# Performance work log

Measured on AMD Instinct MI355X. Metric: run time of the kernel, lower is better.

The kernel has to match this reference:

```python
import jax, jax.numpy as jnp
import numpy as np

EXPERT_NUM = 8
TOPK = 2
N_EMBD = 768
D_FF = 3072
B, S = 2, 1024
T = B * S


def setup_inputs() -> dict:
    key = jax.random.key(0)
    ks = jax.random.split(key, 6)
    x = jax.random.normal(ks[0], (B, S, N_EMBD), dtype=jnp.float32)
    # gumbel noise, matching gumbel_noise(n, k) in the torch module
    u = jax.random.uniform(ks[1], (T, EXPERT_NUM), dtype=jnp.float32,
                           minval=1e-6, maxval=1.0 - 1e-6)
    noise = -jnp.log(-jnp.log(u))
    router_w = jax.random.normal(ks[2], (EXPERT_NUM, N_EMBD), dtype=jnp.float32) * (N_EMBD ** -0.5)
    w1 = jax.random.normal(ks[3], (EXPERT_NUM, N_EMBD, D_FF), dtype=jnp.float32) * (N_EMBD ** -0.5)
    b1 = jnp.zeros((EXPERT_NUM, D_FF), dtype=jnp.float32)
    w2 = jax.random.normal(ks[4], (EXPERT_NUM, D_FF, N_EMBD), dtype=jnp.float32) * (D_FF ** -0.5)
    b2 = jnp.zeros((EXPERT_NUM, N_EMBD), dtype=jnp.float32)
    return {"x": x, "noise": noise, "router_w": router_w,
            "w1": w1, "b1": b1, "w2": w2, "b2": b2}


def reference(x, noise, router_w, w1, b1, w2, b2):
    d = x.shape[-1]
    xs = x.reshape(-1, d)                                   # [T, d]
    gate_logits = xs @ router_w.T + noise                   # [T, E]
    # topk_exp > 1 branch: topk first, then softmax over the k kept logits
    weights, selected = jax.lax.top_k(gate_logits, TOPK)    # [T, k]
    weights = jax.nn.softmax(weights.astype(jnp.float32), axis=1).astype(x.dtype)
    out = jnp.zeros_like(xs)
    for e in range(EXPERT_NUM):
        # combine weight of expert e per token (0 where not selected)
        w_e = jnp.sum(jnp.where(selected == e, weights, 0.0), axis=1)  # [T]
        h = jax.nn.gelu(xs @ w1[e] + b1[e])                 # [T, d_ff]
        y = h @ w2[e] + b2[e]                               # [T, d]
        out = out + w_e[:, None] * y
    return out.reshape(x.shape)
```

## Files before the change

kernel.cpp:

```cpp
#include <hip/hip_runtime.h>
#include <hip/hip_bf16.h>

#define T_TOK 2048
#define NE 768
#define DFF 3072
#define NEXP 8
#define ROWS_PAD 4480
#define MAX_TILES 40

typedef __attribute__((ext_vector_type(8))) __bf16 bf16x8;
typedef __attribute__((ext_vector_type(4))) __bf16 bf16x4;
typedef __attribute__((ext_vector_type(4))) float f32x4;

__device__ __forceinline__ float gelu_tanh(float v) {
  float u = 0.7978845608028654f * (v + 0.044715f * v * v * v);
  float e = __expf(-2.0f * fabsf(u));
  float t = (1.0f - e) / (1.0f + e);
  t = copysignf(t, u);
  return 0.5f * v * (1.0f + t);
}

__global__ void router_kernel(const float* __restrict__ x,
                              const float* __restrict__ noise,
                              const float* __restrict__ rw,
                              int* __restrict__ sel, float* __restrict__ wgt) {
  int tok  = (blockIdx.x * blockDim.x + threadIdx.x) >> 6;
  int lane = threadIdx.x & 63;
  const float* xr = x + (size_t)tok * NE;
  float acc[NEXP];
#pragma unroll
  for (int e = 0; e < NEXP; e++) acc[e] = 0.f;
  for (int d = lane; d < NE; d += 64) {
    float xv = xr[d];
#pragma unroll
    for (int e = 0; e < NEXP; e++) acc[e] += xv * rw[e * NE + d];
  }
#pragma unroll
  for (int e = 0; e < NEXP; e++) {
#pragma unroll
    for (int off = 32; off > 0; off >>= 1) acc[e] += __shfl_xor(acc[e], off);
  }
  if (lane == 0) {
    float lg[NEXP];
#pragma unroll
    for (int e = 0; e < NEXP; e++) lg[e] = acc[e] + noise[tok * NEXP + e];
    int i0 = 0;
#pragma unroll
    for (int e = 1; e < NEXP; e++) if (lg[e] > lg[i0]) i0 = e;
    int i1 = (i0 == 0) ? 1 : 0;
#pragma unroll
    for (int e = 0; e < NEXP; e++) if (e != i0 && lg[e] > lg[i1]) i1 = e;
    float ex = __expf(lg[i1] - lg[i0]);
    float w0 = 1.f / (1.f + ex);
    sel[tok * 2]     = i0; sel[tok * 2 + 1] = i1;
    wgt[tok * 2]     = w0; wgt[tok * 2 + 1] = 1.f - w0;
  }
}

__global__ void assign_kernel(const int* __restrict__ sel,
                              int* __restrict__ offs, int* __restrict__ pair_tok,
                              int* __restrict__ slot_of, int* __restrict__ tiles,
                              int* __restrict__ ntl) {
  __shared__ int scnt[NEXP];
  __shared__ int soff[NEXP + 1];
  int e = threadIdx.x >> 6;
  int lane = threadIdx.x & 63;

  int count = 0;
  for (int t0 = 0; t0 < T_TOK; t0 += 64) {
    int t = t0 + lane;
    bool m = (sel[t * 2] == e) | (sel[t * 2 + 1] == e);
    count += __popcll(__ballot(m));
  }
  if (lane == 0) scnt[e] = count;
  __syncthreads();

  if (threadIdx.x == 0) {
    int s = 0;
    for (int k = 0; k < NEXP; k++) { soff[k] = s; s += scnt[k]; }
    soff[NEXP] = s;
    for (int i = 0; i <= NEXP; i++) offs[i] = soff[i];
    int k2 = 0;
    for (int k = 0; k < NEXP; k++)
      for (int r = soff[k]; r < soff[k + 1]; r += 128) {
        tiles[k2 * 2] = k; tiles[k2 * 2 + 1] = r; k2++;
      }
    *ntl = k2;
  }
  __syncthreads();

  int base = soff[e];
  for (int t0 = 0; t0 < T_TOK; t0 += 64) {
    int t = t0 + lane;
    int s0 = sel[t * 2], s1 = sel[t * 2 + 1];
    bool m0 = (s0 == e), m1 = (s1 == e);
    bool m = m0 | m1;
    unsigned long long mask = __ballot(m);
    int pos = __popcll(mask & ((1ull << lane) - 1ull));
    if (m) {
      int slot = base + pos;
      pair_tok[slot] = t;
      slot_of[t * 2 + (m0 ? 0 : 1)] = slot;
    }
    base += __popcll(mask);
  }
}

__global__ void gather_kernel(const float* __restrict__ x, const int* __restrict__ pair_tok,
                              __hip_bfloat16* __restrict__ xg) {
  int r = blockIdx.x;
  int tok = pair_tok[r];
  const float4* s = (const float4*)(x + (size_t)tok * NE);
  __hip_bfloat16* d = xg + (size_t)r * NE;
  int t = threadIdx.x;
  if (t < NE / 4) {
    float4 v = s[t];
    bf16x4 o;
    o[0] = (__bf16)__float2bfloat16(v.x); o[1] = (__bf16)__float2bfloat16(v.y);
    o[2] = (__bf16)__float2bfloat16(v.z); o[3] = (__bf16)__float2bfloat16(v.w);
    *reinterpret_cast<bf16x4*>(&d[t * 4]) = o;
  }
}

__global__ void transpose_cvt(const float* __restrict__ src, __hip_bfloat16* __restrict__ dst,
                              int K, int N) {
  __shared__ __hip_bfloat16 tile[64 * 72];
  int ntk = K >> 6, ntn = N >> 6;
  int bid = blockIdx.x;
  int e = bid / (ntk * ntn);
  int rem = bid % (ntk * ntn);
  int tk = rem / ntn, tn = rem % ntn;
  const float* s = src + (size_t)e * K * N + (size_t)(tk * 64) * N + tn * 64;
  int t = threadIdx.x;
  int a = t & 15;
  int kp = t >> 4;
#pragma unroll
  for (int i = 0; i < 2; i++) {
    int k = 2 * kp + 32 * i;
    float4 v0 = *reinterpret_cast<const float4*>(&s[(size_t)k * N + 4 * a]);
    float4 v1 = *reinterpret_cast<const float4*>(&s[(size_t)(k + 1) * N + 4 * a]);
    const float* p0 = &v0.x; const float* p1 = &v1.x;
#pragma unroll
    for (int j = 0; j < 4; j++) {
      __hip_bfloat162 p;
      p.x = __float2bfloat16(p0[j]); p.y = __float2bfloat16(p1[j]);
      *reinterpret_cast<__hip_bfloat162*>(&tile[(4 * a + j) * 72 + k]) = p;
    }
  }
  __syncthreads();
  int n = t >> 3, g = t & 7;
  __hip_bfloat16* d = dst + (size_t)e * N * K + (size_t)(tn * 64) * K + tk * 64;
#pragma unroll
  for (int i = 0; i < 2; i++) {
    int row = n + 32 * i;
    bf16x8 v = *reinterpret_cast<const bf16x8*>(&tile[row * 72 + g * 8]);
    *reinterpret_cast<bf16x8*>(&d[(size_t)row * K + g * 8]) = v;
  }
}

template <int K, int N, int MODE, int SPLITS>
__global__ __launch_bounds__(256) void ffn_gemm(
    const __hip_bfloat16* __restrict__ A, const __hip_bfloat16* __restrict__ Bt,
    const float* __restrict__ bias, __hip_bfloat16* __restrict__ DST,
    const int* __restrict__ offs, const int* __restrict__ tiles,
    const int* __restrict__ ntl) {
  constexpr int NT = N / 128;
  constexpr int KS = K / SPLITS;
  constexpr int NS = KS / 64;
  constexpr int NWG = MAX_TILES * SPLITS * NT;

  int b = blockIdx.x;
  int l = (b & 7) * (NWG >> 3) + (b >> 3);
  int ti = l % MAX_TILES;
  int r1 = l / MAX_TILES;
  int sp = r1 % SPLITS;
  int nt = r1 / SPLITS;
  if (ti >= *ntl) return;
  int e = tiles[ti * 2], row0 = tiles[ti * 2 + 1];
  int rend = offs[e + 1];
  int n0 = nt * 128;
  int kbeg = sp * KS;

  __shared__ __align__(16) __hip_bfloat16 lds[2][2][128 * 64];

  int tid = threadIdx.x;
  int w = tid >> 6, l64 = tid & 63;
  int wr = w >> 1, wc = w & 1;
  int r16 = l64 & 15, q = l64 >> 4;
  int swz = r16 & 7;

  f32x4 acc[4][4];
#pragma unroll
  for (int m = 0; m < 4; m++)
#pragma unroll
    for (int n = 0; n < 4; n++) acc[m][n] = (f32x4){0.f, 0.f, 0.f, 0.f};

  const __hip_bfloat16* Bte = Bt + (size_t)e * N * K;

  auto STAGE = [&](int bsel, int k0) {
    char* cA = (char*)lds[bsel][0];
    char* cB = (char*)lds[bsel][1];
#pragma unroll
    for (int i = 0; i < 4; i++) {
      int c = tid + 256 * i;
      int row = c >> 3, p = c & 7;
      const __hip_bfloat16* ga =
          A + (size_t)(row0 + row) * K + k0 + ((p ^ (row & 7)) << 3);
      __builtin_amdgcn_global_load_lds(
          (const __attribute__((address_space(1))) void*)ga,
          (__attribute__((address_space(3))) void*)(cA + c * 16), 16, 0, 0);
    }
#pragma unroll
    for (int i = 0; i < 4; i++) {
      int c = tid + 256 * i;
      int row = c >> 3, p = c & 7;
      const __hip_bfloat16* gb =
          Bte + (size_t)(n0 + row) * K + k0 + ((p ^ (row & 7)) << 3);
      __builtin_amdgcn_global_load_lds(
          (const __attribute__((address_space(1))) void*)gb,
          (__attribute__((address_space(3))) void*)(cB + c * 16), 16, 0, 0);
    }
  };

  STAGE(0, kbeg);
  for (int t = 0; t < NS; t++) {
    if (t + 1 < NS) {
      STAGE((t + 1) & 1, kbeg + (t + 1) * 64);
      asm volatile("s_waitcnt vmcnt(8)" ::: "memory");
    } else {
      asm volatile("s_waitcnt vmcnt(0)" ::: "memory");
    }
    __builtin_amdgcn_s_barrier();
    __builtin_amdgcn_sched_barrier(0);
    const char* cA = (const char*)lds[t & 1][0];
    const char* cB = (const char*)lds[t & 1][1];
#pragma unroll
    for (int kk = 0; kk < 2; kk++) {
      int inner = ((kk * 4 + q) ^ swz) << 4;
      bf16x8 aF[4], bF[4];
#pragma unroll
      for (int m = 0; m < 4; m++)
        aF[m] = *reinterpret_cast<const bf16x8*>(cA + (wr * 64 + m * 16 + r16) * 128 + inner);
#pragma unroll
      for (int n = 0; n < 4; n++)
        bF[n] = *reinterpret_cast<const bf16x8*>(cB + (wc * 64 + n * 16 + r16) * 128 + inner);
#pragma unroll
      for (int m = 0; m < 4; m++)
#pragma unroll
        for (int n = 0; n < 4; n++)
          acc[m][n] = __builtin_amdgcn_mfma_f32_16x16x32_bf16(aF[m], bF[n], acc[m][n], 0, 0, 0);
    }
    __builtin_amdgcn_s_barrier();
  }

  float* ldsF = (float*)&lds[0][0][0];
  __hip_bfloat16* dst = DST + (size_t)sp * ROWS_PAD * N;
#pragma unroll
  for (int hh = 0; hh < 2; hh++) {
    __syncthreads();
    if (wr == hh) {
#pragma unroll
      for (int m = 0; m < 4; m++)
#pragma unroll
        for (int n = 0; n < 4; n++)
#pragma unroll
          for (int rg = 0; rg < 4; rg++)
            ldsF[(m * 16 + q * 4 + rg) * 132 + wc * 64 + n * 16 + r16] = acc[m][n][rg];
    }
    __syncthreads();
#pragma unroll
    for (int i = 0; i < 4; i++) {
      int s = tid + 256 * i;
      int r = s >> 4, c8 = s & 15;
      int rr = row0 + hh * 64 + r;
      if (rr < rend) {
        const float* src = &ldsF[r * 132 + c8 * 8];
        float4 v0 = *reinterpret_cast<const float4*>(src);
        float4 v1 = *reinterpret_cast<const float4*>(src + 4);
        const float* bp = &bias[e * N + n0 + c8 * 8];
        float4 bb0 = *reinterpret_cast<const float4*>(bp);
        float4 bb1 = *reinterpret_cast<const float4*>(bp + 4);
        float vv[8]  = {v0.x, v0.y, v0.z, v0.w, v1.x, v1.y, v1.z, v1.w};
        float bbv[8] = {bb0.x, bb0.y, bb0.z, bb0.w, bb1.x, bb1.y, bb1.z, bb1.w};
        bf16x8 o;
#pragma unroll
        for (int j = 0; j < 8; j++) {
          float val;
          if (MODE == 0) val = gelu_tanh(vv[j] + bbv[j]);
          else           val = vv[j] + (sp == 0 ? bbv[j] : 0.f);
          o[j] = (__bf16)__float2bfloat16(val);
        }
        *reinterpret_cast<bf16x8*>(&dst[(size_t)rr * N + n0 + c8 * 8]) = o;
      }
    }
  }
}

template <int SPLITS>
__global__ void combine_kernel(const __hip_bfloat16* __restrict__ yb,
                               const int* __restrict__ slot_of,
                               const float* __restrict__ wgt,
                               float* __restrict__ out) {
  int t = blockIdx.x;
  int d = threadIdx.x;
  int s0 = slot_of[2 * t], s1 = slot_of[2 * t + 1];
  float w0 = wgt[2 * t], w1 = wgt[2 * t + 1];
  float a0 = 0.f, a1 = 0.f, a2 = 0.f, a3 = 0.f;
#pragma unroll
  for (int sp = 0; sp < SPLITS; sp++) {
    bf16x4 p = reinterpret_cast<const bf16x4*>(yb + (size_t)(sp * ROWS_PAD + s0) * NE)[d];
    bf16x4 r = reinterpret_cast<const bf16x4*>(yb + (size_t)(sp * ROWS_PAD + s1) * NE)[d];
    a0 += w0 * (float)p[0] + w1 * (float)r[0];
    a1 += w0 * (float)p[1] + w1 * (float)r[1];
    a2 += w0 * (float)p[2] + w1 * (float)r[2];
    a3 += w0 * (float)p[3] + w1 * (float)r[3];
  }
  float4 o = {a0, a1, a2, a3};
  reinterpret_cast<float4*>(out)[(size_t)t * (NE / 4) + d] = o;
}

extern "C" void kernel_launch(void* const* d_in, const int* in_sizes, int n_in,
                              void* d_out, int out_size, void* d_ws, size_t ws_size,
                              hipStream_t stream) {
  const float* x     = (const float*)d_in[0];
  const float* noise = (const float*)d_in[1];
  const float* rw    = (const float*)d_in[2];
  const float* w1    = (const float*)d_in[3];
  const float* b1    = (const float*)d_in[4];
  const float* w2    = (const float*)d_in[5];
  const float* b2    = (const float*)d_in[6];
  float* out = (float*)d_out;

  constexpr int SP2 = 2;

  char* ws = (char*)d_ws;
  size_t off = 0;
  auto carve = [&](size_t bytes) { void* p = ws + off; off = (off + bytes + 255) & ~255ull; return p; };
  int*   offs     = (int*)carve((NEXP + 1) * 4);
  int*   sel      = (int*)carve(T_TOK * 2 * 4);
  float* wgt      = (float*)carve(T_TOK * 2 * 4);
  int*   pair_tok = (int*)carve(ROWS_PAD * 4);
  int*   slot_of  = (int*)carve(T_TOK * 2 * 4);
  int*   tiles    = (int*)carve(MAX_TILES * 2 * 4);
  int*   ntl      = (int*)carve(4);
  __hip_bfloat16* xg  = (__hip_bfloat16*)carve((size_t)ROWS_PAD * NE * 2);
  __hip_bfloat16* h   = (__hip_bfloat16*)carve((size_t)ROWS_PAD * DFF * 2);
  __hip_bfloat16* yb  = (__hip_bfloat16*)carve((size_t)SP2 * ROWS_PAD * NE * 2);
  __hip_bfloat16* wt  = (__hip_bfloat16*)carve((size_t)NEXP * NE * DFF * 2);

  if (off > ws_size) {
    hipMemsetAsync(d_out, 0, (size_t)out_size * sizeof(float), stream);
    return;
  }

  router_kernel<<<(T_TOK * 64) / 256, 256, 0, stream>>>(x, noise, rw, sel, wgt);
  assign_kernel<<<1, 512, 0, stream>>>(sel, offs, pair_tok, slot_of, tiles, ntl);
  gather_kernel<<<T_TOK * 2, 256, 0, stream>>>(x, pair_tok, xg);

  transpose_cvt<<<NEXP * (NE / 64) * (DFF / 64), 256, 0, stream>>>(w1, wt, NE, DFF);
  ffn_gemm<NE, DFF, 0, 1><<<MAX_TILES * 1 * (DFF / 128), 256, 0, stream>>>(
      xg, wt, b1, h, offs, tiles, ntl);

  transpose_cvt<<<NEXP * (DFF / 64) * (NE / 64), 256, 0, stream>>>(w2, wt, DFF, NE);
  ffn_gemm<DFF, NE, 1, SP2><<<MAX_TILES * SP2 * (NE / 128), 256, 0, stream>>>(
      h, wt, b2, yb, offs, tiles, ntl);

  combine_kernel<SP2><<<T_TOK, 192, 0, stream>>>(yb, slot_of, wgt, out);
}
```

Before: 146.9 us.

## Fuse weight fp32-to-bf16 transpose into expert GEMM B-operand loading

Removes the separate transpose_cvt kernels that converted and transposed w1 and w2 into a bf16 workspace before each GEMM. The GEMM now reads fp32 weights directly into registers, converts and transposes them in-thread, and writes swizzled bf16 into LDS, software-pipelined against the MFMA loop. It also drops the XCD-aware block remapping. This saves two launches and a full weight round trip through memory, but each GEMM tile now rereads fp32 weights (twice the bytes) once per token tile, adds register pressure and conversion ALU work, and gives up async global_load_lds for the B operand.

Result: slower. 160.4 us (+9.2%).

```diff
diff --git a/kernel.cpp b/kernel.cpp
--- a/kernel.cpp
+++ b/kernel.cpp
@@ -122,57 +122,18 @@
   }
 }
 
-__global__ void transpose_cvt(const float* __restrict__ src, __hip_bfloat16* __restrict__ dst,
-                              int K, int N) {
-  __shared__ __hip_bfloat16 tile[64 * 72];
-  int ntk = K >> 6, ntn = N >> 6;
-  int bid = blockIdx.x;
-  int e = bid / (ntk * ntn);
-  int rem = bid % (ntk * ntn);
-  int tk = rem / ntn, tn = rem % ntn;
-  const float* s = src + (size_t)e * K * N + (size_t)(tk * 64) * N + tn * 64;
-  int t = threadIdx.x;
-  int a = t & 15;
-  int kp = t >> 4;
-#pragma unroll
-  for (int i = 0; i < 2; i++) {
-    int k = 2 * kp + 32 * i;
-    float4 v0 = *reinterpret_cast<const float4*>(&s[(size_t)k * N + 4 * a]);
-    float4 v1 = *reinterpret_cast<const float4*>(&s[(size_t)(k + 1) * N + 4 * a]);
-    const float* p0 = &v0.x; const float* p1 = &v1.x;
-#pragma unroll
-    for (int j = 0; j < 4; j++) {
-      __hip_bfloat162 p;
-      p.x = __float2bfloat16(p0[j]); p.y = __float2bfloat16(p1[j]);
-      *reinterpret_cast<__hip_bfloat162*>(&tile[(4 * a + j) * 72 + k]) = p;
-    }
-  }
-  __syncthreads();
-  int n = t >> 3, g = t & 7;
-  __hip_bfloat16* d = dst + (size_t)e * N * K + (size_t)(tn * 64) * K + tk * 64;
-#pragma unroll
-  for (int i = 0; i < 2; i++) {
-    int row = n + 32 * i;
-    bf16x8 v = *reinterpret_cast<const bf16x8*>(&tile[row * 72 + g * 8]);
-    *reinterpret_cast<bf16x8*>(&d[(size_t)row * K + g * 8]) = v;
-  }
-}
-
 template <int K, int N, int MODE, int SPLITS>
-__global__ __launch_bounds__(256) void ffn_gemm(
-    const __hip_bfloat16* __restrict__ A, const __hip_bfloat16* __restrict__ Bt,
+__global__ __launch_bounds__(256) void ffn_gemm_f(
+    const __hip_bfloat16* __restrict__ A, const float* __restrict__ W,
     const float* __restrict__ bias, __hip_bfloat16* __restrict__ DST,
     const int* __restrict__ offs, const int* __restrict__ tiles,
     const int* __restrict__ ntl) {
   constexpr int NT = N / 128;
   constexpr int KS = K / SPLITS;
   constexpr int NS = KS / 64;
-  constexpr int NWG = MAX_TILES * SPLITS * NT;
-
-  int b = blockIdx.x;
-  int l = (b & 7) * (NWG >> 3) + (b >> 3);
-  int ti = l % MAX_TILES;
-  int r1 = l / MAX_TILES;
+  int bid = blockIdx.x;
+  int ti = bid % MAX_TILES;
+  int r1 = bid / MAX_TILES;
   int sp = r1 % SPLITS;
   int nt = r1 / SPLITS;
   if (ti >= *ntl) return;
@@ -189,17 +150,19 @@
   int r16 = l64 & 15, q = l64 >> 4;
   int swz = r16 & 7;
 
+  int K8 = tid >> 5;
+  int n4 = (tid & 31) * 4;
+
   f32x4 acc[4][4];
 #pragma unroll
   for (int m = 0; m < 4; m++)
 #pragma unroll
     for (int n = 0; n < 4; n++) acc[m][n] = (f32x4){0.f, 0.f, 0.f, 0.f};
 
-  const __hip_bfloat16* Bte = Bt + (size_t)e * N * K;
-
-  auto STAGE = [&](int bsel, int k0) {
+  const float* We = W + (size_t)e * K * N;
+
+  auto ISSUE_A = [&](int bsel, int k0) {
     char* cA = (char*)lds[bsel][0];
-    char* cB = (char*)lds[bsel][1];
 #pragma unroll
     for (int i = 0; i < 4; i++) {
       int c = tid + 256 * i;
@@ -210,30 +173,44 @@
           (const __attribute__((address_space(1))) void*)ga,
           (__attribute__((address_space(3))) void*)(cA + c * 16), 16, 0, 0);
     }
-#pragma unroll
-    for (int i = 0; i < 4; i++) {
-      int c = tid + 256 * i;
-      int row = c >> 3, p = c & 7;
-      const __hip_bfloat16* gb =
-          Bte + (size_t)(n0 + row) * K + k0 + ((p ^ (row & 7)) << 3);
-      __builtin_amdgcn_global_load_lds(
-          (const __attribute__((address_space(1))) void*)gb,
-          (__attribute__((address_space(3))) void*)(cB + c * 16), 16, 0, 0);
-    }
   };
 
-  STAGE(0, kbeg);
+  float4 vf[8];
+  auto LOAD_B = [&](int k0) {
+#pragma unroll
+    for (int kk = 0; kk < 8; kk++)
+      vf[kk] = *reinterpret_cast<const float4*>(
+          &We[(size_t)(k0 + K8 * 8 + kk) * N + n0 + n4]);
+  };
+  auto WRITE_B = [&](int bsel) {
+    char* cB = (char*)lds[bsel][1];
+#pragma unroll
+    for (int j = 0; j < 4; j++) {
+      bf16x8 pk;
+      const float* vp = (const float*)vf;
+#pragma unroll
+      for (int kk = 0; kk < 8; kk++)
+        pk[kk] = (__bf16)__float2bfloat16(vp[kk * 4 + j]);
+      int row = n4 + j;
+      int chunk = row * 8 + (K8 ^ (row & 7));
+      *reinterpret_cast<bf16x8*>(cB + chunk * 16) = pk;
+    }
+  };
+
+  ISSUE_A(0, kbeg);
+  LOAD_B(kbeg);
+  WRITE_B(0);
+  __syncthreads();
+
   for (int t = 0; t < NS; t++) {
-    if (t + 1 < NS) {
-      STAGE((t + 1) & 1, kbeg + (t + 1) * 64);
-      asm volatile("s_waitcnt vmcnt(8)" ::: "memory");
-    } else {
-      asm volatile("s_waitcnt vmcnt(0)" ::: "memory");
-    }
-    __builtin_amdgcn_s_barrier();
-    __builtin_amdgcn_sched_barrier(0);
-    const char* cA = (const char*)lds[t & 1][0];
-    const char* cB = (const char*)lds[t & 1][1];
+    const int cur = t & 1, nxt = cur ^ 1;
+    const bool more = (t + 1 < NS);
+    if (more) {
+      ISSUE_A(nxt, kbeg + (t + 1) * 64);
+      LOAD_B(kbeg + (t + 1) * 64);
+    }
+    const char* cA = (const char*)lds[cur][0];
+    const char* cB = (const char*)lds[cur][1];
 #pragma unroll
     for (int kk = 0; kk < 2; kk++) {
       int inner = ((kk * 4 + q) ^ swz) << 4;
@@ -250,7 +227,8 @@
         for (int n = 0; n < 4; n++)
           acc[m][n] = __builtin_amdgcn_mfma_f32_16x16x32_bf16(aF[m], bF[n], acc[m][n], 0, 0, 0);
     }
-    __builtin_amdgcn_s_barrier();
+    if (more) WRITE_B(nxt);
+    __syncthreads();
   }
 
   float* ldsF = (float*)&lds[0][0][0];
@@ -346,7 +324,6 @@
   __hip_bfloat16* xg  = (__hip_bfloat16*)carve((size_t)ROWS_PAD * NE * 2);
   __hip_bfloat16* h   = (__hip_bfloat16*)carve((size_t)ROWS_PAD * DFF * 2);
   __hip_bfloat16* yb  = (__hip_bfloat16*)carve((size_t)SP2 * ROWS_PAD * NE * 2);
-  __hip_bfloat16* wt  = (__hip_bfloat16*)carve((size_t)NEXP * NE * DFF * 2);
 
   if (off > ws_size) {
     hipMemsetAsync(d_out, 0, (size_t)out_size * sizeof(float), stream);
@@ -357,13 +334,11 @@
   assign_kernel<<<1, 512, 0, stream>>>(sel, offs, pair_tok, slot_of, tiles, ntl);
   gather_kernel<<<T_TOK * 2, 256, 0, stream>>>(x, pair_tok, xg);
 
-  transpose_cvt<<<NEXP * (NE / 64) * (DFF / 64), 256, 0, stream>>>(w1, wt, NE, DFF);
-  ffn_gemm<NE, DFF, 0, 1><<<MAX_TILES * 1 * (DFF / 128), 256, 0, stream>>>(
-      xg, wt, b1, h, offs, tiles, ntl);
-
-  transpose_cvt<<<NEXP * (DFF / 64) * (NE / 64), 256, 0, stream>>>(w2, wt, DFF, NE);
-  ffn_gemm<DFF, NE, 1, SP2><<<MAX_TILES * SP2 * (NE / 128), 256, 0, stream>>>(
-      h, wt, b2, yb, offs, tiles, ntl);
+  ffn_gemm_f<NE, DFF, 0, 1><<<MAX_TILES * 1 * (DFF / 128), 256, 0, stream>>>(
+      xg, w1, b1, h, offs, tiles, ntl);
+
+  ffn_gemm_f<DFF, NE, 1, SP2><<<MAX_TILES * SP2 * (NE / 128), 256, 0, stream>>>(
+      h, w2, b2, yb, offs, tiles, ntl);
 
   combine_kernel<SP2><<<T_TOK, 192, 0, stream>>>(yb, slot_of, wgt, out);
 }
```
